# Optimization experiments

Hardware: AMD Instinct MI355X
Metric: run time of the kernel (lower is better)

Reference implementation:

```python
import jax, jax.numpy as jnp
import numpy as np

N_HEAD = 16

def _ln(x, g, b):
    m = jnp.mean(x, axis=-1, keepdims=True)
    v = jnp.var(x, axis=-1, keepdims=True)
    return (x - m) / jnp.sqrt(v + 1e-5) * g + b

def setup_inputs() -> dict:
    key = jax.random.key(0)
    B, T, D, L, V = 2, 1024, 1024, 4, 32000
    ks = jax.random.split(key, 8)
    s = 0.02
    return {
        'input_ids': jax.random.randint(ks[0], (B, T), 0, V),
        'wte': jax.random.normal(ks[1], (V, D), jnp.float32) * s,
        'wpe': jax.random.normal(ks[2], (T, D), jnp.float32) * s,
        'ln1_g': jnp.ones((L, D), jnp.float32), 'ln1_b': jnp.zeros((L, D), jnp.float32),
        'w_qkv': jax.random.normal(ks[3], (L, D, 3 * D), jnp.float32) * s,
        'b_qkv': jnp.zeros((L, 3 * D), jnp.float32),
        'w_proj': jax.random.normal(ks[4], (L, D, D), jnp.float32) * s,
        'b_proj': jnp.zeros((L, D), jnp.float32),
        'ln2_g': jnp.ones((L, D), jnp.float32), 'ln2_b': jnp.zeros((L, D), jnp.float32),
        'w_fc1': jax.random.normal(ks[5], (L, D, 4 * D), jnp.float32) * s,
        'b_fc1': jnp.zeros((L, 4 * D), jnp.float32),
        'w_fc2': jax.random.normal(ks[6], (L, 4 * D, D), jnp.float32) * s,
        'b_fc2': jnp.zeros((L, D), jnp.float32),
        'lnf_g': jnp.ones((D,), jnp.float32), 'lnf_b': jnp.zeros((D,), jnp.float32),
        'w_lm': jax.random.normal(ks[7], (D, V), jnp.float32) * s,
    }

def reference(input_ids, wte, wpe, ln1_g, ln1_b, w_qkv, b_qkv, w_proj, b_proj,
              ln2_g, ln2_b, w_fc1, b_fc1, w_fc2, b_fc2, lnf_g, lnf_b, w_lm):
    B, T = input_ids.shape
    D = wte.shape[1]
    H = N_HEAD
    hd = D // H
    mask = jnp.tril(jnp.ones((T, T), dtype=bool))  # causal
    x = wte[input_ids] + wpe[:T][None, :, :]  # token + position embeddings

    def layer(h, p):
        g1, bb1, Wq, bq, Wp, bp, g2, bb2, W1, b1, W2, b2 = p
        a = _ln(h, g1, bb1)
        qkv = a @ Wq + bq
        q, k, v = jnp.split(qkv, 3, axis=-1)
        q = q.reshape(B, T, H, hd)
        k = k.reshape(B, T, H, hd)
        v = v.reshape(B, T, H, hd)
        att = jnp.einsum('bqhd,bkhd->bhqk', q, k) / jnp.sqrt(jnp.float32(hd))
        att = jnp.where(mask[None, None], att, -jnp.inf)
        att = jax.nn.softmax(att, axis=-1)
        y = jnp.einsum('bhqk,bkhd->bqhd', att, v).reshape(B, T, D)
        h = h + y @ Wp + bp
        m = _ln(h, g2, bb2)
        # torch nn.GELU default is exact erf variant
        m = jax.nn.gelu(m @ W1 + b1, approximate=False) @ W2 + b2
        h = h + m
        return h, None

    params = (ln1_g, ln1_b, w_qkv, b_qkv, w_proj, b_proj,
              ln2_g, ln2_b, w_fc1, b_fc1, w_fc2, b_fc2)
    h, _ = jax.lax.scan(layer, x, params)
    h = _ln(h, lnf_g, lnf_b)
    logits = h @ w_lm  # [B, T, vocab]
    return logits
```

## Files before the change

kernel.cpp:

```cpp
#include <hip/hip_runtime.h>
#include <hip/hip_bf16.h>
#include <math.h>

typedef __attribute__((ext_vector_type(4))) float f32x4;
typedef __attribute__((ext_vector_type(8))) short short8;
typedef __attribute__((ext_vector_type(4))) unsigned short ushort4v;

__device__ __forceinline__ unsigned short f2bf(float f) {
    return __builtin_bit_cast(unsigned short, __float2bfloat16(f));
}

__device__ __forceinline__ void gload16(const void* g, void* l) {
    __builtin_amdgcn_global_load_lds(
        (const __attribute__((address_space(1))) unsigned int*)g,
        (__attribute__((address_space(3))) unsigned int*)l, 16, 0, 0);
}

#define WAITV6() asm volatile("s_waitcnt vmcnt(6)" ::: "memory")
#define WAITV0() asm volatile("s_waitcnt vmcnt(0)" ::: "memory")

__global__ __launch_bounds__(256)
void tc_kernel(const float* __restrict__ in, __hip_bfloat16* __restrict__ out,
               int N, int K)
{
    __shared__ float tile[64][65];
    const size_t loff = (size_t)blockIdx.z * K * N;
    const int k0 = blockIdx.x * 64, n0 = blockIdx.y * 64;
    const int t = threadIdx.x;
    {
        int kk = t >> 2, nb = (t & 3) * 16;
        const float* src = in + loff + (size_t)(k0 + kk) * N + n0 + nb;
        #pragma unroll
        for (int j = 0; j < 4; ++j) {
            float4 v = *(const float4*)(src + j * 4);
            tile[kk][nb + j*4 + 0] = v.x; tile[kk][nb + j*4 + 1] = v.y;
            tile[kk][nb + j*4 + 2] = v.z; tile[kk][nb + j*4 + 3] = v.w;
        }
    }
    __syncthreads();
    {
        int nn = t >> 2, kb = (t & 3) * 16;
        __hip_bfloat16* dst = out + loff + (size_t)(n0 + nn) * K + k0 + kb;
        short8 w0, w1;
        #pragma unroll
        for (int j = 0; j < 8; ++j) w0[j] = (short)f2bf(tile[kb + j][nn]);
        #pragma unroll
        for (int j = 0; j < 8; ++j) w1[j] = (short)f2bf(tile[kb + 8 + j][nn]);
        *(short8*)dst = w0;
        *(short8*)(dst + 8) = w1;
    }
}

__global__ __launch_bounds__(256)
void embed_kernel(const int* __restrict__ ids, const float* __restrict__ wte,
                  const float* __restrict__ wpe, float* __restrict__ h)
{
    int row  = blockIdx.x;
    int tpos = row & 1023;
    int id   = ids[row];
    float4 a = ((const float4*)(wte + (size_t)id * 1024))[threadIdx.x];
    float4 p = ((const float4*)(wpe + (size_t)tpos * 1024))[threadIdx.x];
    float4 o; o.x = a.x + p.x; o.y = a.y + p.y; o.z = a.z + p.z; o.w = a.w + p.w;
    ((float4*)(h + (size_t)row * 1024))[threadIdx.x] = o;
}

__global__ __launch_bounds__(256)
void ln_kernel(const float* __restrict__ x, const float* __restrict__ g,
               const float* __restrict__ b, __hip_bfloat16* __restrict__ out)
{
    size_t row = blockIdx.x;
    float4 v = ((const float4*)(x + row * 1024))[threadIdx.x];
    float s  = v.x + v.y + v.z + v.w;
    float s2 = v.x*v.x + v.y*v.y + v.z*v.z + v.w*v.w;
    #pragma unroll
    for (int off = 32; off; off >>= 1) {
        s  += __shfl_xor(s, off);
        s2 += __shfl_xor(s2, off);
    }
    __shared__ float rs[4], rs2[4];
    int wave = threadIdx.x >> 6;
    if ((threadIdx.x & 63) == 0) { rs[wave] = s; rs2[wave] = s2; }
    __syncthreads();
    s  = rs[0] + rs[1] + rs[2] + rs[3];
    s2 = rs2[0] + rs2[1] + rs2[2] + rs2[3];
    float mean = s * (1.f / 1024.f);
    float var  = s2 * (1.f / 1024.f) - mean * mean;
    float rstd = rsqrtf(var + 1e-5f);
    float4 gg = ((const float4*)g)[threadIdx.x];
    float4 bb = ((const float4*)b)[threadIdx.x];
    ushort4v ov;
    ov[0] = f2bf((v.x - mean) * rstd * gg.x + bb.x);
    ov[1] = f2bf((v.y - mean) * rstd * gg.y + bb.y);
    ov[2] = f2bf((v.z - mean) * rstd * gg.z + bb.z);
    ov[3] = f2bf((v.w - mean) * rstd * gg.w + bb.w);
    ((ushort4v*)(out + row * 1024))[threadIdx.x] = ov;
}

template<bool OUT_BF16, bool GELU_ACT, bool NT>
__global__ __launch_bounds__(256)
void gemm_bf16(const __hip_bfloat16* __restrict__ A,
               const __hip_bfloat16* __restrict__ Bt,
               const float* __restrict__ bias, const float* __restrict__ resid,
               void* __restrict__ Cout, int M, int N, int K, int GN)
{
    __shared__ unsigned char smem[73728];
    int mblk, pnl;
    {
        int bid = blockIdx.x;
        int x = bid & 7, j = bid >> 3;
        int pw = GN >> 3;
        int whole = pw * 128;
        if (bid < whole) { pnl = x + 8 * (j >> 4); mblk = j & 15; }
        else { int r = bid - whole; pnl = (pw << 3) + (r >> 4); mblk = r & 15; }
    }
    const int m0 = mblk * 128;
    const int n0 = pnl * 64;
    const int t    = threadIdx.x;
    const int lane = t & 63;
    const int wave = t >> 6;
    const int wm = (wave & 1) * 64;
    const int wn = (wave >> 1) * 32;

    f32x4 acc[4][2];
    #pragma unroll
    for (int i = 0; i < 4; ++i)
        #pragma unroll
        for (int j = 0; j < 2; ++j) {
            acc[i][j][0] = 0.f; acc[i][j][1] = 0.f; acc[i][j][2] = 0.f; acc[i][j][3] = 0.f;
        }

    const int l8 = lane >> 3;
    const int lc = (lane & 7) ^ l8;
    const __hip_bfloat16* agp[4];
    const __hip_bfloat16* bgp[2];
    int aoff[4];
    int boff[2];
    #pragma unroll
    for (int i = 0; i < 4; ++i) {
        int row = wave * 32 + i * 8 + l8;
        agp[i]  = A + (size_t)(m0 + row) * K + lc * 8;
        aoff[i] = (wave * 32 + i * 8) * 128;
    }
    #pragma unroll
    for (int i = 0; i < 2; ++i) {
        int row = wave * 16 + i * 8 + l8;
        bgp[i]  = Bt + (size_t)(n0 + row) * K + lc * 8;
        boff[i] = (wave * 16 + i * 8) * 128;
    }

    int a0 = 0,     a1 = 16384, a2 = 32768;
    int b0 = 49152, b1 = 57344, b2 = 65536;

    #pragma unroll
    for (int i = 0; i < 4; ++i) gload16(agp[i], smem + a0 + aoff[i]);
    #pragma unroll
    for (int i = 0; i < 2; ++i) gload16(bgp[i], smem + b0 + boff[i]);
    if (64 < K) {
        #pragma unroll
        for (int i = 0; i < 4; ++i) gload16(agp[i] + 64, smem + a1 + aoff[i]);
        #pragma unroll
        for (int i = 0; i < 2; ++i) gload16(bgp[i] + 64, smem + b1 + boff[i]);
    }

    for (int k0 = 0; k0 < K; k0 += 64) {
        if (k0 + 64 < K) { WAITV6(); } else { WAITV0(); }
        __builtin_amdgcn_s_barrier();
        if (k0 + 128 < K) {
            #pragma unroll
            for (int i = 0; i < 4; ++i) gload16(agp[i] + k0 + 128, smem + a2 + aoff[i]);
            #pragma unroll
            for (int i = 0; i < 2; ++i) gload16(bgp[i] + k0 + 128, smem + b2 + boff[i]);
        }
        const unsigned char* abuf = smem + a0;
        const unsigned char* bbuf = smem + b0;
        const int lr = lane & 15;
        const int lk = lane >> 4;
        #pragma unroll
        for (int ks = 0; ks < 2; ++ks) {
            int chunk = ks * 4 + lk;
            short8 af[4], bfr[2];
            #pragma unroll
            for (int m = 0; m < 4; ++m) {
                int row = wm + m * 16 + lr;
                af[m] = *(const short8*)(abuf + row * 128 + ((chunk * 16) ^ ((row & 7) << 4)));
            }
            #pragma unroll
            for (int n = 0; n < 2; ++n) {
                int nn = wn + n * 16 + lr;
                bfr[n] = *(const short8*)(bbuf + nn * 128 + ((chunk * 16) ^ ((nn & 7) << 4)));
            }
            #pragma unroll
            for (int m = 0; m < 4; ++m)
                #pragma unroll
                for (int n = 0; n < 2; ++n)
                    acc[m][n] = __builtin_amdgcn_mfma_f32_16x16x32_bf16(af[m], bfr[n], acc[m][n], 0, 0, 0);
        }
        int ta = a0; a0 = a1; a1 = a2; a2 = ta;
        int tb = b0; b0 = b1; b1 = b2; b2 = tb;
    }

    const int lr = lane & 15;
    const int lq = lane >> 4;
    float bv[2];
    #pragma unroll
    for (int n = 0; n < 2; ++n)
        bv[n] = bias ? bias[n0 + wn + n * 16 + lr] : 0.f;
    #pragma unroll
    for (int m = 0; m < 4; ++m) {
        int rbase = m0 + wm + m * 16 + lq * 4;
        #pragma unroll
        for (int j = 0; j < 4; ++j) {
            int row = rbase + j;
            #pragma unroll
            for (int n = 0; n < 2; ++n) {
                int col = n0 + wn + n * 16 + lr;
                float v = acc[m][n][j] + bv[n];
                if (resid) v += resid[(size_t)row * N + col];
                if (GELU_ACT) v = 0.5f * v * (1.f + erff(v * 0.70710678118654752f));
                if (OUT_BF16) {
                    ((__hip_bfloat16*)Cout)[(size_t)row * N + col] = __float2bfloat16(v);
                } else if (NT) {
                    __builtin_nontemporal_store(v, (float*)Cout + (size_t)row * N + col);
                } else {
                    ((float*)Cout)[(size_t)row * N + col] = v;
                }
            }
        }
    }
}

__global__ __launch_bounds__(256)
void attn_mfma(const __hip_bfloat16* __restrict__ qkv,
               __hip_bfloat16* __restrict__ y)
{
    __shared__ short Qs[64][72];
    __shared__ short Ps[64][72];
    __shared__ unsigned char Kl[8192];
    __shared__ short Vt[64][72];

    const int bid = blockIdx.x;
    const int p   = bid >> 5;
    const int qt  = (p < 8) ? (15 - 2 * p) : (2 * (p - 8));
    const int bh  = bid & 31;
    const int b = bh >> 4, h = bh & 15;
    const int t = threadIdx.x, lane = t & 63, w = t >> 6;
    const int lr = lane & 15, lg = lane >> 4;
    const size_t base = (size_t)b * 1024 * 3072;
    const int qbase = qt * 64;

    {
        int row = t >> 2, c = t & 3;
        const short8* qsrc = (const short8*)(qkv + base + (size_t)(qbase + row) * 3072 + h * 64);
        *(short8*)&Qs[row][c * 8]      = qsrc[c];
        *(short8*)&Qs[row][c * 8 + 32] = qsrc[c + 4];
    }
    __syncthreads();

    short8 aq0 = *(const short8*)&Qs[w * 16 + lr][0 * 32 + lg * 8];
    short8 aq1 = *(const short8*)&Qs[w * 16 + lr][1 * 32 + lg * 8];

    f32x4 oacc[4];
    #pragma unroll
    for (int dt = 0; dt < 4; ++dt) { oacc[dt][0]=0.f; oacc[dt][1]=0.f; oacc[dt][2]=0.f; oacc[dt][3]=0.f; }
    float lsum[4] = {0.f, 0.f, 0.f, 0.f};

    const int ntiles = qt + 1;
    const int kkey = t >> 2, kc = t & 3;
    const int vkey = t & 63, vc = t >> 6;

    short8 rk0, rk1, rv0, rv1;
    {
        const short8* ksrc = (const short8*)(qkv + base + (size_t)kkey * 3072 + 1024 + h * 64);
        rk0 = ksrc[kc]; rk1 = ksrc[kc + 4];
        const short8* vsrc = (const short8*)(qkv + base + (size_t)vkey * 3072 + 2048 + h * 64);
        rv0 = vsrc[vc]; rv1 = vsrc[vc + 4];
    }
    {
        int rb = kkey * 128, sw = (kkey & 7) << 4;
        *(short8*)(Kl + rb + ((kc * 16) ^ sw)) = rk0;
        *(short8*)(Kl + rb + (((kc + 4) * 16) ^ sw)) = rk1;
        #pragma unroll
        for (int j = 0; j < 8; ++j) Vt[vc * 8 + j][vkey] = rv0[j];
        #pragma unroll
        for (int j = 0; j < 8; ++j) Vt[(vc + 4) * 8 + j][vkey] = rv1[j];
    }
    __syncthreads();

    for (int tile = 0; tile < ntiles; ++tile) {
        if (tile + 1 < ntiles) {
            const int kb2 = (tile + 1) * 64;
            const short8* ksrc = (const short8*)(qkv + base + (size_t)(kb2 + kkey) * 3072 + 1024 + h * 64);
            rk0 = ksrc[kc]; rk1 = ksrc[kc + 4];
            const short8* vsrc = (const short8*)(qkv + base + (size_t)(kb2 + vkey) * 3072 + 2048 + h * 64);
            rv0 = vsrc[vc]; rv1 = vsrc[vc + 4];
        }

        const int kb = tile * 64;
        f32x4 sacc[4];
        #pragma unroll
        for (int kt = 0; kt < 4; ++kt) { sacc[kt][0]=0.f; sacc[kt][1]=0.f; sacc[kt][2]=0.f; sacc[kt][3]=0.f; }
        #pragma unroll
        for (int ks = 0; ks < 2; ++ks) {
            short8 aq = ks ? aq1 : aq0;
            #pragma unroll
            for (int kt = 0; kt < 4; ++kt) {
                int krow = kt * 16 + lr;
                short8 bk = *(const short8*)(Kl + krow * 128 + (((ks * 4 + lg) * 16) ^ ((krow & 7) << 4)));
                sacc[kt] = __builtin_amdgcn_mfma_f32_16x16x32_bf16(aq, bk, sacc[kt], 0, 0, 0);
            }
        }

        #pragma unroll
        for (int kt = 0; kt < 4; ++kt) {
            int key = kb + kt * 16 + lr;
            #pragma unroll
            for (int j = 0; j < 4; ++j) {
                int q = qbase + w * 16 + lg * 4 + j;
                float pv = (key <= q) ? __expf(sacc[kt][j] * 0.125f) : 0.f;
                lsum[j] += pv;
                Ps[w * 16 + lg * 4 + j][kt * 16 + lr] = (short)f2bf(pv);
            }
        }

        #pragma unroll
        for (int ks = 0; ks < 2; ++ks) {
            short8 ap = *(const short8*)&Ps[w * 16 + lr][ks * 32 + lg * 8];
            #pragma unroll
            for (int dt = 0; dt < 4; ++dt) {
                short8 bv = *(const short8*)&Vt[dt * 16 + lr][ks * 32 + lg * 8];
                oacc[dt] = __builtin_amdgcn_mfma_f32_16x16x32_bf16(ap, bv, oacc[dt], 0, 0, 0);
            }
        }

        if (tile + 1 < ntiles) {
            __syncthreads();
            int rb = kkey * 128, sw = (kkey & 7) << 4;
            *(short8*)(Kl + rb + ((kc * 16) ^ sw)) = rk0;
            *(short8*)(Kl + rb + (((kc + 4) * 16) ^ sw)) = rk1;
            #pragma unroll
            for (int j = 0; j < 8; ++j) Vt[vc * 8 + j][vkey] = rv0[j];
            #pragma unroll
            for (int j = 0; j < 8; ++j) Vt[(vc + 4) * 8 + j][vkey] = rv1[j];
            __syncthreads();
        }
    }

    #pragma unroll
    for (int j = 0; j < 4; ++j) {
        float l = lsum[j];
        l += __shfl_xor(l, 1); l += __shfl_xor(l, 2);
        l += __shfl_xor(l, 4); l += __shfl_xor(l, 8);
        float inv = 1.f / l;
        int qrow = qbase + w * 16 + lg * 4 + j;
        __hip_bfloat16* dst = y + (size_t)(b * 1024 + qrow) * 1024 + h * 64;
        #pragma unroll
        for (int dt = 0; dt < 4; ++dt)
            dst[dt * 16 + lr] = __float2bfloat16(oacc[dt][j] * inv);
    }
}

extern "C" void kernel_launch(void* const* d_in, const int* in_sizes, int n_in,
                              void* d_out, int out_size, void* d_ws, size_t ws_size,
                              hipStream_t stream)
{
    (void)in_sizes; (void)n_in; (void)out_size; (void)ws_size;

    const int*   ids    = (const int*)d_in[0];
    const float* wte    = (const float*)d_in[1];
    const float* wpe    = (const float*)d_in[2];
    const float* ln1_g  = (const float*)d_in[3];
    const float* ln1_b  = (const float*)d_in[4];
    const float* w_qkv  = (const float*)d_in[5];
    const float* b_qkv  = (const float*)d_in[6];
    const float* w_proj = (const float*)d_in[7];
    const float* b_proj = (const float*)d_in[8];
    const float* ln2_g  = (const float*)d_in[9];
    const float* ln2_b  = (const float*)d_in[10];
    const float* w_fc1  = (const float*)d_in[11];
    const float* b_fc1  = (const float*)d_in[12];
    const float* w_fc2  = (const float*)d_in[13];
    const float* b_fc2  = (const float*)d_in[14];
    const float* lnf_g  = (const float*)d_in[15];
    const float* lnf_b  = (const float*)d_in[16];
    const float* w_lm   = (const float*)d_in[17];

    char* ws = (char*)d_ws;
    __hip_bfloat16* abuf_bf = (__hip_bfloat16*)ws;
    float*          hbuf    = (float*)(ws + (4u<<20));
    __hip_bfloat16* qkvb_bf = (__hip_bfloat16*)(ws + (12u<<20));
    __hip_bfloat16* ybuf_bf = (__hip_bfloat16*)(ws + (24u<<20));
    __hip_bfloat16* mbuf_bf = (__hip_bfloat16*)(ws + (28u<<20));
    __hip_bfloat16* wlm_bf  = (__hip_bfloat16*)(ws + (4u<<20));

    __hip_bfloat16* wq_bf = (__hip_bfloat16*)d_out;
    __hip_bfloat16* wp_bf = wq_bf + (size_t)4*1024*3072;
    __hip_bfloat16* w1_bf = wp_bf + (size_t)4*1024*1024;
    __hip_bfloat16* w2_bf = w1_bf + (size_t)4*1024*4096;

    float* out = (float*)d_out;

    tc_kernel<<<dim3(16, 48, 4), 256, 0, stream>>>(w_qkv,  wq_bf, 3072, 1024);
    tc_kernel<<<dim3(16, 16, 4), 256, 0, stream>>>(w_proj, wp_bf, 1024, 1024);
    tc_kernel<<<dim3(16, 64, 4), 256, 0, stream>>>(w_fc1,  w1_bf, 4096, 1024);
    tc_kernel<<<dim3(64, 16, 4), 256, 0, stream>>>(w_fc2,  w2_bf, 1024, 4096);

    embed_kernel<<<2048, 256, 0, stream>>>(ids, wte, wpe, hbuf);

    for (int l = 0; l < 4; ++l) {
        ln_kernel<<<2048, 256, 0, stream>>>(hbuf, ln1_g + l*1024, ln1_b + l*1024, abuf_bf);
        gemm_bf16<true,false,false><<<16*48, 256, 0, stream>>>(
            abuf_bf, wq_bf + (size_t)l*1024*3072, b_qkv + l*3072, nullptr, qkvb_bf, 2048, 3072, 1024, 48);
        attn_mfma<<<512, 256, 0, stream>>>(qkvb_bf, ybuf_bf);
        gemm_bf16<false,false,false><<<16*16, 256, 0, stream>>>(
            ybuf_bf, wp_bf + (size_t)l*1024*1024, b_proj + l*1024, hbuf, hbuf, 2048, 1024, 1024, 16);
        ln_kernel<<<2048, 256, 0, stream>>>(hbuf, ln2_g + l*1024, ln2_b + l*1024, abuf_bf);
        gemm_bf16<true,true,false><<<16*64, 256, 0, stream>>>(
            abuf_bf, w1_bf + (size_t)l*1024*4096, b_fc1 + l*4096, nullptr, mbuf_bf, 2048, 4096, 1024, 64);
        gemm_bf16<false,false,false><<<16*16, 256, 0, stream>>>(
            mbuf_bf, w2_bf + (size_t)l*4096*1024, b_fc2 + l*1024, hbuf, hbuf, 2048, 1024, 4096, 16);
    }

    ln_kernel<<<2048, 256, 0, stream>>>(hbuf, lnf_g, lnf_b, abuf_bf);
    tc_kernel<<<dim3(16, 500, 1), 256, 0, stream>>>(w_lm, wlm_bf, 32000, 1024);
    gemm_bf16<false,false,true><<<16*500, 256, 0, stream>>>(
        abuf_bf, wlm_bf, nullptr, nullptr, out, 2048, 32000, 1024, 500);
}
```

Measured before the change: 850.3 us.

## Use dedicated double-buffered 128x128 tile GEMM for LM head

Adds a separate LM-head GEMM kernel that uses 128x128 output tiles instead of 128x64, with double-buffered LDS staging via global_load_lds and nontemporal fp32 stores. Larger N tiles halve the number of blocks and reuse each loaded A tile across twice as many columns, cutting redundant A traffic for the 32000-wide vocab projection. The generic GEMM loses its nontemporal template flag and is renamed. The cost is higher per-wave accumulator register pressure (16 MFMA tiles), which may lower occupancy, and the two-stage buffering may not fully hide load latency.

```diff
diff --git a/kernel.cpp b/kernel.cpp
--- a/kernel.cpp
+++ b/kernel.cpp
@@ -96,12 +96,12 @@
     ((ushort4v*)(out + row * 1024))[threadIdx.x] = ov;
 }
 
-template<bool OUT_BF16, bool GELU_ACT, bool NT>
+template<bool OUT_BF16, bool GELU_ACT>
 __global__ __launch_bounds__(256)
-void gemm_bf16(const __hip_bfloat16* __restrict__ A,
-               const __hip_bfloat16* __restrict__ Bt,
-               const float* __restrict__ bias, const float* __restrict__ resid,
-               void* __restrict__ Cout, int M, int N, int K, int GN)
+void gemm_p3(const __hip_bfloat16* __restrict__ A,
+             const __hip_bfloat16* __restrict__ Bt,
+             const float* __restrict__ bias, const float* __restrict__ resid,
+             void* __restrict__ Cout, int M, int N, int K, int GN)
 {
     __shared__ unsigned char smem[73728];
     int mblk, pnl;
@@ -217,13 +217,120 @@
                 float v = acc[m][n][j] + bv[n];
                 if (resid) v += resid[(size_t)row * N + col];
                 if (GELU_ACT) v = 0.5f * v * (1.f + erff(v * 0.70710678118654752f));
-                if (OUT_BF16) {
+                if (OUT_BF16)
                     ((__hip_bfloat16*)Cout)[(size_t)row * N + col] = __float2bfloat16(v);
-                } else if (NT) {
-                    __builtin_nontemporal_store(v, (float*)Cout + (size_t)row * N + col);
-                } else {
+                else
                     ((float*)Cout)[(size_t)row * N + col] = v;
-                }
+            }
+        }
+    }
+}
+
+__global__ __launch_bounds__(256)
+void gemm_db_nt(const __hip_bfloat16* __restrict__ A,
+                const __hip_bfloat16* __restrict__ Bt,
+                float* __restrict__ Cout, int M, int N, int K, int GN)
+{
+    __shared__ unsigned char smem[65536];
+    int mblk, pnl;
+    {
+        int bid = blockIdx.x;
+        int x = bid & 7, j = bid >> 3;
+        int pw = GN >> 3;
+        int whole = pw * 128;
+        if (bid < whole) { pnl = x + 8 * (j >> 4); mblk = j & 15; }
+        else { int r = bid - whole; pnl = (pw << 3) + (r >> 4); mblk = r & 15; }
+    }
+    const int m0 = mblk * 128;
+    const int n0 = pnl * 128;
+    const int t    = threadIdx.x;
+    const int lane = t & 63;
+    const int wave = t >> 6;
+    const int wm = (wave >> 1) * 64;
+    const int wn = (wave & 1) * 64;
+
+    f32x4 acc[4][4];
+    #pragma unroll
+    for (int i = 0; i < 4; ++i)
+        #pragma unroll
+        for (int j = 0; j < 4; ++j) {
+            acc[i][j][0] = 0.f; acc[i][j][1] = 0.f; acc[i][j][2] = 0.f; acc[i][j][3] = 0.f;
+        }
+
+    const int l8 = lane >> 3;
+    const int lc = (lane & 7) ^ l8;
+    const __hip_bfloat16* agp[4];
+    const __hip_bfloat16* bgp[4];
+    int aoff[4];
+    int boff[4];
+    #pragma unroll
+    for (int i = 0; i < 4; ++i) {
+        int row = wave * 32 + i * 8 + l8;
+        agp[i]  = A + (size_t)(m0 + row) * K + lc * 8;
+        aoff[i] = (wave * 32 + i * 8) * 128;
+        bgp[i]  = Bt + (size_t)(n0 + row) * K + lc * 8;
+        boff[i] = (wave * 32 + i * 8) * 128;
+    }
+    const int aBufOff[2] = { 0, 16384 };
+    const int bBufOff[2] = { 32768, 49152 };
+
+    #pragma unroll
+    for (int i = 0; i < 4; ++i) gload16(agp[i], smem + aBufOff[0] + aoff[i]);
+    #pragma unroll
+    for (int i = 0; i < 4; ++i) gload16(bgp[i], smem + bBufOff[0] + boff[i]);
+    __syncthreads();
+
+    int cur = 0;
+    for (int k0 = 0; k0 < K; k0 += 64) {
+        if (k0 + 64 < K) {
+            #pragma unroll
+            for (int i = 0; i < 4; ++i)
+                gload16(agp[i] + k0 + 64, smem + aBufOff[cur ^ 1] + aoff[i]);
+            #pragma unroll
+            for (int i = 0; i < 4; ++i)
+                gload16(bgp[i] + k0 + 64, smem + bBufOff[cur ^ 1] + boff[i]);
+        }
+        const unsigned char* abuf = smem + aBufOff[cur];
+        const unsigned char* bbuf = smem + bBufOff[cur];
+        const int lr = lane & 15;
+        const int lk = lane >> 4;
+        #pragma unroll
+        for (int ks = 0; ks < 2; ++ks) {
+            int chunk = ks * 4 + lk;
+            short8 af[4], bfr[4];
+            #pragma unroll
+            for (int m = 0; m < 4; ++m) {
+                int row = wm + m * 16 + lr;
+                af[m] = *(const short8*)(abuf + row * 128 + ((chunk * 16) ^ ((row & 7) << 4)));
+            }
+            #pragma unroll
+            for (int n = 0; n < 4; ++n) {
+                int nn = wn + n * 16 + lr;
+                bfr[n] = *(const short8*)(bbuf + nn * 128 + ((chunk * 16) ^ ((nn & 7) << 4)));
+            }
+            #pragma unroll
+            for (int m = 0; m < 4; ++m)
+                #pragma unroll
+                for (int n = 0; n < 4; ++n)
+                    acc[m][n] = __builtin_amdgcn_mfma_f32_16x16x32_bf16(af[m], bfr[n], acc[m][n], 0, 0, 0);
+        }
+        __syncthreads();
+        cur ^= 1;
+    }
+
+    const int lr = lane & 15;
+    const int lq = lane >> 4;
+    #pragma unroll
+    for (int m = 0; m < 4; ++m) {
+        int rbase = m0 + wm + m * 16 + lq * 4;
+        #pragma unroll
+        for (int j = 0; j < 4; ++j) {
+            int row = rbase + j;
+            #pragma unroll
+            for (int n = 0; n < 4; ++n) {
+                int col = n0 + wn + n * 16 + lr;
+                __builtin_nontemporal_store(acc[m][n][j],
+                    Cout + (size_t)row * N + col);
             }
         }
     }
@@ -408,20 +515,20 @@
 
     for (int l = 0; l < 4; ++l) {
         ln_kernel<<<2048, 256, 0, stream>>>(hbuf, ln1_g + l*1024, ln1_b + l*1024, abuf_bf);
-        gemm_bf16<true,false,false><<<16*48, 256, 0, stream>>>(
+        gemm_p3<true,false><<<16*48, 256, 0, stream>>>(
             abuf_bf, wq_bf + (size_t)l*1024*3072, b_qkv + l*3072, nullptr, qkvb_bf, 2048, 3072, 1024, 48);
         attn_mfma<<<512, 256, 0, stream>>>(qkvb_bf, ybuf_bf);
-        gemm_bf16<false,false,false><<<16*16, 256, 0, stream>>>(
+        gemm_p3<false,false><<<16*16, 256, 0, stream>>>(
             ybuf_bf, wp_bf + (size_t)l*1024*1024, b_proj + l*1024, hbuf, hbuf, 2048, 1024, 1024, 16);
         ln_kernel<<<2048, 256, 0, stream>>>(hbuf, ln2_g + l*1024, ln2_b + l*1024, abuf_bf);
-        gemm_bf16<true,true,false><<<16*64, 256, 0, stream>>>(
+        gemm_p3<true,true><<<16*64, 256, 0, stream>>>(
             abuf_bf, w1_bf + (size_t)l*1024*4096, b_fc1 + l*4096, nullptr, mbuf_bf, 2048, 4096, 1024, 64);
-        gemm_bf16<false,false,false><<<16*16, 256, 0, stream>>>(
+        gemm_p3<false,false><<<16*16, 256, 0, stream>>>(
             mbuf_bf, w2_bf + (size_t)l*4096*1024, b_fc2 + l*1024, hbuf, hbuf, 2048, 1024, 4096, 16);
     }
 
     ln_kernel<<<2048, 256, 0, stream>>>(hbuf, lnf_g, lnf_b, abuf_bf);
     tc_kernel<<<dim3(16, 500, 1), 256, 0, stream>>>(w_lm, wlm_bf, 32000, 1024);
-    gemm_bf16<false,false,true><<<16*500, 256, 0, stream>>>(
-        abuf_bf, wlm_bf, nullptr, nullptr, out, 2048, 32000, 1024, 500);
-}
+    gemm_db_nt<<<16*250, 256, 0, stream>>>(
+        abuf_bf, wlm_bf, out, 2048, 32000, 1024, 250);
+}
```

Result: faster. 819.8 us (-3.6%).
